# Kernel tuning notes

Hardware: AMD Instinct MI355X
Metric: run time of the kernel (lower is better)

## Reference

```python
import jax, jax.numpy as jnp
import numpy as np

DECAY = 0.8
EPS = 1e-05


def setup_inputs() -> dict:
    key = jax.random.key(0)
    k_x, k_e = jax.random.split(key)
    x = jax.random.normal(k_x, (8, 4096, 256), dtype=jnp.float32)
    embed = jax.random.normal(k_e, (8192, 256), dtype=jnp.float32)
    cluster_size = jnp.zeros((8192,), dtype=jnp.float32)
    embed_avg = embed  # buffer initialized as embed.clone()
    return {"x": x, "embed": embed, "cluster_size": cluster_size, "embed_avg": embed_avg}


def reference(x, embed, cluster_size, embed_avg):
    shape = x.shape
    K, d = embed.shape
    flatten = x.reshape(-1, d)  # [N, d]

    dist = -(jnp.sum(flatten * flatten, axis=1, keepdims=True)
             - 2.0 * (flatten @ embed.T)
             + jnp.sum(embed * embed, axis=1)[None, :])  # [N, K]
    embed_ind = jnp.argmax(dist, axis=-1)  # [N]

    quantize = jnp.take(embed, embed_ind, axis=0).reshape(shape)
    embed_ind_out = embed_ind.reshape(shape[:-1])

    # Training-mode EMA update (one_hot sum / one_hot matmul expressed as scatter-adds)
    counts = jnp.zeros((K,), dtype=x.dtype).at[embed_ind].add(1.0)  # embed_onehot.sum(0)
    embed_sum = jnp.zeros((K, d), dtype=x.dtype).at[embed_ind].add(flatten)  # (flatten^T @ onehot)^T

    new_cluster_size = cluster_size * DECAY + counts * (1.0 - DECAY)
    new_embed_avg = embed_avg * DECAY + embed_sum * (1.0 - DECAY)

    smoothed = (new_cluster_size + EPS) / (new_cluster_size.sum() + K * EPS) * new_cluster_size.sum()
    new_embed = new_embed_avg / smoothed[:, None]

    return quantize, embed_ind_out, new_cluster_size, new_embed_avg, new_embed
```

## Files before the change

kernel.cpp:

```cpp
#include <hip/hip_runtime.h>

#define N_ROWS 32768
#define DIM    256
#define KCODES 8192
#define DECAYF 0.8f
#define OMDF   0.2f
#define EPSF   1e-5f

#define Q_OFF    0
#define IND_OFF  8388608
#define CS_OFF   8421376
#define EA_OFF   8429568
#define NE_OFF   10526720


#define WS_E2    0
#define WS_CNT   8192
#define WS_START 16384
#define WS_CUR   24576
#define WS_SUM   40960

typedef _Float16 half8 __attribute__((ext_vector_type(8)));
typedef float floatx16 __attribute__((ext_vector_type(16)));

#define GLOAD16(g, l) __builtin_amdgcn_global_load_lds( \
    (const __attribute__((address_space(1))) void*)(g), \
    (__attribute__((address_space(3))) void*)(l), 16, 0, 0)

#define PREP_ROWS 32
__global__ void prep_all_kernel(const float* __restrict__ x,
                                const float* __restrict__ embed,
                                const float* __restrict__ cs,
                                _Float16* __restrict__ Xp,
                                _Float16* __restrict__ Ep,
                                float* __restrict__ out,
                                float* __restrict__ ws) {
  __shared__ __align__(16) _Float16 L[PREP_ROWS][264];
  __shared__ float red[4];
  const int t = threadIdx.x;
  const int bid = blockIdx.x;

  if (bid < 1024) {
    if (bid < 128) {
      unsigned long long* gbest = (unsigned long long*)(out + EA_OFF);
      gbest[bid * 256 + t] = 0ULL;
    } else if (bid < 160) {
      ((int*)(ws + WS_CNT))[(bid - 128) * 256 + t] = 0;
    }
    const int row0 = bid * PREP_ROWS;
    #pragma unroll
    for (int it = 0; it < 8; ++it) {
      int idx = it * 256 + t;
      int r = idx >> 6, q = idx & 63;
      float4 v = *(const float4*)&x[(size_t)(row0 + r) * DIM + q * 4];
      L[r][q * 4 + 0] = (_Float16)v.x;
      L[r][q * 4 + 1] = (_Float16)v.y;
      L[r][q * 4 + 2] = (_Float16)v.z;
      L[r][q * 4 + 3] = (_Float16)v.w;
    }
    __syncthreads();
    #pragma unroll
    for (int it = 0; it < 4; ++it) {
      int idx = it * 256 + t;
      int slot = idx >> 5, r = idx & 31;
      *(float4*)&Xp[((size_t)slot * N_ROWS + row0 + r) * 8] =
          *(const float4*)&L[r][slot * 8];
    }
  } else {
    const int row0 = (bid - 1024) * PREP_ROWS;
    float* e2 = ws + WS_E2;
    #pragma unroll
    for (int it = 0; it < 8; ++it) {
      int idx = it * 256 + t;
      int r = idx >> 6, q = idx & 63;
      float4 v = *(const float4*)&embed[(size_t)(row0 + r) * DIM + q * 4];
      L[r][q * 4 + 0] = (_Float16)v.x;
      L[r][q * 4 + 1] = (_Float16)v.y;
      L[r][q * 4 + 2] = (_Float16)v.z;
      L[r][q * 4 + 3] = (_Float16)v.w;
      float ssq = v.x * v.x + v.y * v.y + v.z * v.z + v.w * v.w;
      #pragma unroll
      for (int o = 32; o; o >>= 1) ssq += __shfl_xor(ssq, o);
      if ((t & 63) == 0) e2[row0 + r] = ssq;
    }
    if (bid == 1024) {
      float s = 0.0f;
      for (int j = t; j < KCODES; j += 256) s += cs[j];
      #pragma unroll
      for (int o = 32; o; o >>= 1) s += __shfl_xor(s, o);
      if ((t & 63) == 0) red[t >> 6] = s;
    }
    __syncthreads();
    if (bid == 1024 && t == 0)
      ws[WS_SUM] = red[0] + red[1] + red[2] + red[3];
    #pragma unroll
    for (int it = 0; it < 4; ++it) {
      int idx = it * 256 + t;
      int slot = idx >> 5, r = idx & 31;
      *(float4*)&Ep[((size_t)slot * KCODES + row0 + r) * 8] =
          *(const float4*)&L[r][slot * 8];
    }
  }
}

__global__ __launch_bounds__(512, 2) void main_kernel(
    const _Float16* __restrict__ Xp, const _Float16* __restrict__ Ep,
    const float* __restrict__ e2, unsigned long long* __restrict__ gbest) {
  __shared__ __align__(16) _Float16 As[4 * 4 * 256 * 8];
  __shared__ __align__(16) _Float16 Bs[4 * 4 * 256 * 8];
  __shared__ __align__(16) float e2s[256];

  const int t = threadIdx.x;
  const int w = t >> 6;
  const int lane = t & 63;
  const int l31 = lane & 31;
  const int h = lane >> 5;
  const int wm = w >> 2;
  const int wn = w & 3;

  const int bid = blockIdx.x;
  const int bi = bid >> 3;
  const int cb = (bid & 7) * 4 + (bi >> 5);
  const int rbg = bi & 31;
  const int codes0 = cb * 256;
  const int rowbase = rbg * 1024;

  const bool isA = (w < 4);
  const int slot = isA ? w : (w - 4);

  const _Float16* estage = Ep + ((size_t)slot * KCODES + codes0 + lane) * 8;
  const _Float16* xstage = Xp + ((size_t)slot * N_ROWS + rowbase + lane) * 8;
  _Float16* adst = &As[slot * 2048];
  _Float16* bdst = &Bs[slot * 2048];

  auto stage = [&](int s) {
    const int buf = s & 3;
    const int se4 = (s & 7) * 4;
    if (isA) {
      const _Float16* src = estage + (size_t)se4 * KCODES * 8;
      _Float16* dst = adst + buf * 8192;
      #pragma unroll
      for (int q = 0; q < 4; ++q)
        GLOAD16(src + q * 512, dst + q * 512);
    } else {
      const _Float16* src =
          xstage + (size_t)se4 * N_ROWS * 8 + (size_t)(s >> 3) * 256 * 8;
      _Float16* dst = bdst + buf * 8192;
      #pragma unroll
      for (int q = 0; q < 4; ++q)
        GLOAD16(src + q * 512, dst + q * 512);
    }
  };

  if (t < 64) {
    float4 v = *(const float4*)&e2[codes0 + t * 4];
    *(float4*)&e2s[t * 4] = v;
  }
  __builtin_amdgcn_sched_barrier(0);
  stage(0);
  stage(1);
  asm volatile("s_waitcnt vmcnt(4)" ::: "memory");
  asm volatile("s_waitcnt lgkmcnt(0)" ::: "memory");
  __builtin_amdgcn_s_barrier();
  __builtin_amdgcn_sched_barrier(0);

  floatx16 acc[4][2];
  unsigned long long pbest[4][2];

  #pragma unroll
  for (int tile = 0; tile < 4; ++tile) {
    #pragma unroll
    for (int ct = 0; ct < 4; ++ct) {
      const int cl = wm * 128 + ct * 32 + 4 * h;
      #pragma unroll
      for (int rq = 0; rq < 4; ++rq) {
        float4 v = *(const float4*)&e2s[cl + rq * 8];
        acc[ct][0][rq * 4 + 0] = -0.5f * v.x;
        acc[ct][0][rq * 4 + 1] = -0.5f * v.y;
        acc[ct][0][rq * 4 + 2] = -0.5f * v.z;
        acc[ct][0][rq * 4 + 3] = -0.5f * v.w;
      }
      acc[ct][1] = acc[ct][0];
    }

    #pragma unroll
    for (int i = 0; i < 8; ++i) {
      const int s = tile * 8 + i;
      if (s + 2 < 32) stage(s + 2);
      __builtin_amdgcn_sched_barrier(0);

      const int cur = (s & 3) * 8192;
      #pragma unroll
      for (int ks = 0; ks < 2; ++ks) {
        const int sbase = cur + (2 * ks + h) * 2048;
        half8 a0 = *(const half8*)&As[sbase + (wm * 128 + l31) * 8];
        half8 a1 = *(const half8*)&As[sbase + (wm * 128 + 32 + l31) * 8];
        half8 a2 = *(const half8*)&As[sbase + (wm * 128 + 64 + l31) * 8];
        half8 a3 = *(const half8*)&As[sbase + (wm * 128 + 96 + l31) * 8];
        half8 b0 = *(const half8*)&Bs[sbase + (wn * 64 + l31) * 8];
        half8 b1 = *(const half8*)&Bs[sbase + (wn * 64 + 32 + l31) * 8];
        __builtin_amdgcn_s_setprio(1);
        acc[0][0] = __builtin_amdgcn_mfma_f32_32x32x16_f16(a0, b0, acc[0][0], 0, 0, 0);
        acc[0][1] = __builtin_amdgcn_mfma_f32_32x32x16_f16(a0, b1, acc[0][1], 0, 0, 0);
        acc[1][0] = __builtin_amdgcn_mfma_f32_32x32x16_f16(a1, b0, acc[1][0], 0, 0, 0);
        acc[1][1] = __builtin_amdgcn_mfma_f32_32x32x16_f16(a1, b1, acc[1][1], 0, 0, 0);
        acc[2][0] = __builtin_amdgcn_mfma_f32_32x32x16_f16(a2, b0, acc[2][0], 0, 0, 0);
        acc[2][1] = __builtin_amdgcn_mfma_f32_32x32x16_f16(a2, b1, acc[2][1], 0, 0, 0);
        acc[3][0] = __builtin_amdgcn_mfma_f32_32x32x16_f16(a3, b0, acc[3][0], 0, 0, 0);
        acc[3][1] = __builtin_amdgcn_mfma_f32_32x32x16_f16(a3, b1, acc[3][1], 0, 0, 0);
        __builtin_amdgcn_s_setprio(0);
      }
      __builtin_amdgcn_sched_barrier(0);

      if (s < 31) {
        if (s < 30) {
          asm volatile("s_waitcnt vmcnt(4)" ::: "memory");
        } else {
          asm volatile("s_waitcnt vmcnt(0)" ::: "memory");
        }
        __builtin_amdgcn_s_barrier();
        __builtin_amdgcn_sched_barrier(0);
      }
    }

    #pragma unroll
    for (int rt = 0; rt < 2; ++rt) {
      float best = -3.0e38f;
      int bidx = 0;
      #pragma unroll
      for (int ct = 0; ct < 4; ++ct) {
        const int cbase = codes0 + wm * 128 + ct * 32 + 4 * h;
        #pragma unroll
        for (int r = 0; r < 16; ++r) {
          const int code = cbase + (r & 3) + 8 * (r >> 2);
          float v = acc[ct][rt][r];
          if (v > best || (v == best && code < bidx)) { best = v; bidx = code; }
        }
      }
      unsigned u = __float_as_uint(best);
      u = (u & 0x80000000u) ? ~u : (u | 0x80000000u);
      unsigned long long p =
          ((unsigned long long)u << 32) | (unsigned)(8191 - bidx);
      unsigned long long op = (unsigned long long)__shfl_xor((long long)p, 32);
      if (op > p) p = op;
      pbest[tile][rt] = p;
    }
  }

  #pragma unroll
  for (int tile = 0; tile < 4; ++tile)
    #pragma unroll
    for (int rt = 0; rt < 2; ++rt)
      if (h == 0)
        atomicMax(&gbest[rowbase + tile * 256 + wn * 64 + rt * 32 + l31],
                  pbest[tile][rt]);
}

__global__ void decode_count_kernel(const unsigned long long* __restrict__ gbest,
                                    float* __restrict__ out,
                                    int* __restrict__ cnt) {
  int r = blockIdx.x * blockDim.x + threadIdx.x;
  unsigned long long p = gbest[r];
  int k = 8191 - (int)(unsigned)(p & 0xFFFFFFFFull);
  out[IND_OFF + r] = (float)k;
  atomicAdd(&cnt[k], 1);
}

__global__ void prefix_kernel(const int* __restrict__ cnt,
                              int* __restrict__ start,
                              int* __restrict__ cursor) {
  __shared__ int part[1024];
  const int t = threadIdx.x;
  int loc[8];
  int s = 0;
  #pragma unroll
  for (int j = 0; j < 8; ++j) { loc[j] = cnt[t * 8 + j]; s += loc[j]; }
  part[t] = s;
  __syncthreads();
  for (int off = 1; off < 1024; off <<= 1) {
    int v = (t >= off) ? part[t - off] : 0;
    __syncthreads();
    part[t] += v;
    __syncthreads();
  }
  int base = part[t] - s;
  #pragma unroll
  for (int j = 0; j < 8; ++j) {
    start[t * 8 + j] = base;
    cursor[t * 8 + j] = base;
    base += loc[j];
  }
}

__global__ void scatter_rows_kernel(const float* __restrict__ out,
                                    int* __restrict__ cursor,
                                    int* __restrict__ rowlist) {
  int r = blockIdx.x * blockDim.x + threadIdx.x;
  int k = (int)out[IND_OFF + r];
  int pos = atomicAdd(&cursor[k], 1);
  rowlist[pos] = r;
}

__global__ void bucket_final_kernel(const float* __restrict__ x,
                                    const float* __restrict__ cs,
                                    const float* __restrict__ embed_avg,
                                    const int* __restrict__ start,
                                    const int* __restrict__ cnt,
                                    const int* __restrict__ rowlist,
                                    float* __restrict__ out,
                                    const float* __restrict__ ws_sum) {
  const int lane = threadIdx.x & 63;
  const int k = blockIdx.x * 4 + (threadIdx.x >> 6);
  const int s = start[k];
  const int n = cnt[k];
  float4 acc = make_float4(0.f, 0.f, 0.f, 0.f);
  int i = 0;
  for (; i + 2 <= n; i += 2) {
    int r0 = rowlist[s + i];
    int r1 = rowlist[s + i + 1];
    float4 v0 = *(const float4*)&x[(size_t)r0 * DIM + lane * 4];
    float4 v1 = *(const float4*)&x[(size_t)r1 * DIM + lane * 4];
    acc.x += v0.x + v1.x; acc.y += v0.y + v1.y;
    acc.z += v0.z + v1.z; acc.w += v0.w + v1.w;
  }
  if (i < n) {
    int r0 = rowlist[s + i];
    float4 v0 = *(const float4*)&x[(size_t)r0 * DIM + lane * 4];
    acc.x += v0.x; acc.y += v0.y; acc.z += v0.z; acc.w += v0.w;
  }
  const float S = DECAYF * (*ws_sum) + OMDF * (float)N_ROWS;
  const float scale = S / (S + (float)KCODES * EPSF);
  float ncs = cs[k] * DECAYF + (float)n * OMDF;
  if (lane == 0) out[CS_OFF + k] = ncs;
  float4 ea = *(const float4*)&embed_avg[(size_t)k * DIM + lane * 4];
  float4 nea;
  nea.x = ea.x * DECAYF + acc.x * OMDF;
  nea.y = ea.y * DECAYF + acc.y * OMDF;
  nea.z = ea.z * DECAYF + acc.z * OMDF;
  nea.w = ea.w * DECAYF + acc.w * OMDF;
  *(float4*)&out[EA_OFF + (size_t)k * DIM + lane * 4] = nea;
  float inv_sm = 1.0f / ((ncs + EPSF) * scale);
  float4 ne;
  ne.x = nea.x * inv_sm;
  ne.y = nea.y * inv_sm;
  ne.z = nea.z * inv_sm;
  ne.w = nea.w * inv_sm;
  *(float4*)&out[NE_OFF + (size_t)k * DIM + lane * 4] = ne;
}

__global__ void finish_q_kernel(const float* __restrict__ embed,
                                float* __restrict__ out) {
  const int lane = threadIdx.x & 63;
  const int wave = (blockIdx.x * blockDim.x + threadIdx.x) >> 6;
  for (int row = wave; row < N_ROWS; row += 2048) {
    int k = (int)out[IND_OFF + row];
    float4 ev = *(const float4*)&embed[(size_t)k * DIM + lane * 4];
    *(float4*)&out[Q_OFF + (size_t)row * DIM + lane * 4] = ev;
  }
}

extern "C" void kernel_launch(void* const* d_in, const int* in_sizes, int n_in,
                              void* d_out, int out_size, void* d_ws, size_t ws_size,
                              hipStream_t stream) {
  const float* x = (const float*)d_in[0];
  const float* embed = (const float*)d_in[1];
  const float* cs = (const float*)d_in[2];
  const float* ea = (const float*)d_in[3];
  float* out = (float*)d_out;
  float* ws = (float*)d_ws;

  float* e2 = ws + WS_E2;
  int* cnt = (int*)(ws + WS_CNT);
  int* start = (int*)(ws + WS_START);
  int* cursor = (int*)(ws + WS_CUR);
  float* ws_sum = ws + WS_SUM;

  _Float16* Xp = (_Float16*)(out + Q_OFF);
  int* rowlist = (int*)(out + Q_OFF + 4194304);
  unsigned long long* gbest = (unsigned long long*)(out + EA_OFF);
  _Float16* Ep = (_Float16*)(out + EA_OFF + 65536);

  prep_all_kernel<<<1280, 256, 0, stream>>>(x, embed, cs, Xp, Ep, out, ws);
  main_kernel<<<1024, 512, 0, stream>>>(Xp, Ep, e2, gbest);
  decode_count_kernel<<<128, 256, 0, stream>>>(gbest, out, cnt);
  prefix_kernel<<<1, 1024, 0, stream>>>(cnt, start, cursor);
  scatter_rows_kernel<<<128, 256, 0, stream>>>(out, cursor, rowlist);
  bucket_final_kernel<<<2048, 256, 0, stream>>>(x, cs, ea, start, cnt,
                                                rowlist, out, ws_sum);
  finish_q_kernel<<<512, 256, 0, stream>>>(embed, out);
}
```

Before: 378.5 us.

## Make distance GEMM blocks persistent over 4096 rows with a continuous prefetch pipeline

Each main_kernel block now covers 4096 rows (16 row tiles, processed in 4 super-groups) instead of 1024, and the grid shrinks from 1024 to 256 blocks. The staging lambda takes an explicit buffer, k-slice and row-tile, so the double-buffered global-to-LDS prefetch runs without a break across row tiles. Atomic argmax updates to gbest are flushed after each group of 4 tiles. The aim is to amortise block start-up costs and pipeline fill/drain, and to avoid a second dispatch wave. The cost is that with one block per CU the kernel runs at half of the allowed occupancy, which leaves fewer waves to hide memory latency.

```diff
diff --git a/kernel.cpp b/kernel.cpp
--- a/kernel.cpp
+++ b/kernel.cpp
@@ -120,10 +120,10 @@
 
   const int bid = blockIdx.x;
   const int bi = bid >> 3;
-  const int cb = (bid & 7) * 4 + (bi >> 5);
-  const int rbg = bi & 31;
+  const int cb = (bid & 7) * 4 + (bi >> 3);
+  const int rbg = bi & 7;
   const int codes0 = cb * 256;
-  const int rowbase = rbg * 1024;
+  const int rowbase = rbg * 4096;
 
   const bool isA = (w < 4);
   const int slot = isA ? w : (w - 4);
@@ -133,18 +133,16 @@
   _Float16* adst = &As[slot * 2048];
   _Float16* bdst = &Bs[slot * 2048];
 
-  auto stage = [&](int s) {
-    const int buf = s & 3;
-    const int se4 = (s & 7) * 4;
+  auto stage = [&](int buf, int se4, int rowT) {
     if (isA) {
-      const _Float16* src = estage + (size_t)se4 * KCODES * 8;
+      const _Float16* src = estage + (size_t)se4 * (KCODES * 8);
       _Float16* dst = adst + buf * 8192;
       #pragma unroll
       for (int q = 0; q < 4; ++q)
         GLOAD16(src + q * 512, dst + q * 512);
     } else {
       const _Float16* src =
-          xstage + (size_t)se4 * N_ROWS * 8 + (size_t)(s >> 3) * 256 * 8;
+          xstage + (size_t)se4 * (N_ROWS * 8) + (size_t)rowT * 2048;
       _Float16* dst = bdst + buf * 8192;
       #pragma unroll
       for (int q = 0; q < 4; ++q)
@@ -157,8 +155,8 @@
     *(float4*)&e2s[t * 4] = v;
   }
   __builtin_amdgcn_sched_barrier(0);
-  stage(0);
-  stage(1);
+  stage(0, 0, 0);
+  stage(1, 4, 0);
   asm volatile("s_waitcnt vmcnt(4)" ::: "memory");
   asm volatile("s_waitcnt lgkmcnt(0)" ::: "memory");
   __builtin_amdgcn_s_barrier();
@@ -167,93 +165,105 @@
   floatx16 acc[4][2];
   unsigned long long pbest[4][2];
 
-  #pragma unroll
-  for (int tile = 0; tile < 4; ++tile) {
-    #pragma unroll
-    for (int ct = 0; ct < 4; ++ct) {
-      const int cl = wm * 128 + ct * 32 + 4 * h;
-      #pragma unroll
-      for (int rq = 0; rq < 4; ++rq) {
-        float4 v = *(const float4*)&e2s[cl + rq * 8];
-        acc[ct][0][rq * 4 + 0] = -0.5f * v.x;
-        acc[ct][0][rq * 4 + 1] = -0.5f * v.y;
-        acc[ct][0][rq * 4 + 2] = -0.5f * v.z;
-        acc[ct][0][rq * 4 + 3] = -0.5f * v.w;
+  #pragma unroll 1
+  for (int sg = 0; sg < 4; ++sg) {
+    #pragma unroll
+    for (int tt = 0; tt < 4; ++tt) {
+      const int rowT = sg * 4 + tt;
+      #pragma unroll
+      for (int ct = 0; ct < 4; ++ct) {
+        const int cl = wm * 128 + ct * 32 + 4 * h;
+        #pragma unroll
+        for (int rq = 0; rq < 4; ++rq) {
+          float4 v = *(const float4*)&e2s[cl + rq * 8];
+          acc[ct][0][rq * 4 + 0] = -0.5f * v.x;
+          acc[ct][0][rq * 4 + 1] = -0.5f * v.y;
+          acc[ct][0][rq * 4 + 2] = -0.5f * v.z;
+          acc[ct][0][rq * 4 + 3] = -0.5f * v.w;
+        }
+        acc[ct][1] = acc[ct][0];
       }
-      acc[ct][1] = acc[ct][0];
-    }
-
-    #pragma unroll
-    for (int i = 0; i < 8; ++i) {
-      const int s = tile * 8 + i;
-      if (s + 2 < 32) stage(s + 2);
-      __builtin_amdgcn_sched_barrier(0);
-
-      const int cur = (s & 3) * 8192;
-      #pragma unroll
-      for (int ks = 0; ks < 2; ++ks) {
-        const int sbase = cur + (2 * ks + h) * 2048;
-        half8 a0 = *(const half8*)&As[sbase + (wm * 128 + l31) * 8];
-        half8 a1 = *(const half8*)&As[sbase + (wm * 128 + 32 + l31) * 8];
-        half8 a2 = *(const half8*)&As[sbase + (wm * 128 + 64 + l31) * 8];
-        half8 a3 = *(const half8*)&As[sbase + (wm * 128 + 96 + l31) * 8];
-        half8 b0 = *(const half8*)&Bs[sbase + (wn * 64 + l31) * 8];
-        half8 b1 = *(const half8*)&Bs[sbase + (wn * 64 + 32 + l31) * 8];
-        __builtin_amdgcn_s_setprio(1);
-        acc[0][0] = __builtin_amdgcn_mfma_f32_32x32x16_f16(a0, b0, acc[0][0], 0, 0, 0);
-        acc[0][1] = __builtin_amdgcn_mfma_f32_32x32x16_f16(a0, b1, acc[0][1], 0, 0, 0);
-        acc[1][0] = __builtin_amdgcn_mfma_f32_32x32x16_f16(a1, b0, acc[1][0], 0, 0, 0);
-        acc[1][1] = __builtin_amdgcn_mfma_f32_32x32x16_f16(a1, b1, acc[1][1], 0, 0, 0);
-        acc[2][0] = __builtin_amdgcn_mfma_f32_32x32x16_f16(a2, b0, acc[2][0], 0, 0, 0);
-        acc[2][1] = __builtin_amdgcn_mfma_f32_32x32x16_f16(a2, b1, acc[2][1], 0, 0, 0);
-        acc[3][0] = __builtin_amdgcn_mfma_f32_32x32x16_f16(a3, b0, acc[3][0], 0, 0, 0);
-        acc[3][1] = __builtin_amdgcn_mfma_f32_32x32x16_f16(a3, b1, acc[3][1], 0, 0, 0);
-        __builtin_amdgcn_s_setprio(0);
-      }
-      __builtin_amdgcn_sched_barrier(0);
-
-      if (s < 31) {
-        if (s < 30) {
-          asm volatile("s_waitcnt vmcnt(4)" ::: "memory");
-        } else {
-          asm volatile("s_waitcnt vmcnt(0)" ::: "memory");
+
+      #pragma unroll
+      for (int i = 0; i < 8; ++i) {
+        const bool lastTile = (sg == 3 && tt == 3);
+        if (!(lastTile && i >= 6)) {
+          const int ip = i + 2;
+          stage(ip & 3, (ip & 7) * 4, rowT + (ip >> 3));
         }
-        __builtin_amdgcn_s_barrier();
         __builtin_amdgcn_sched_barrier(0);
-      }
-    }
-
-    #pragma unroll
-    for (int rt = 0; rt < 2; ++rt) {
-      float best = -3.0e38f;
-      int bidx = 0;
-      #pragma unroll
-      for (int ct = 0; ct < 4; ++ct) {
-        const int cbase = codes0 + wm * 128 + ct * 32 + 4 * h;
+
+        const int cur = (i & 3) * 8192;
         #pragma unroll
-        for (int r = 0; r < 16; ++r) {
-          const int code = cbase + (r & 3) + 8 * (r >> 2);
-          float v = acc[ct][rt][r];
-          if (v > best || (v == best && code < bidx)) { best = v; bidx = code; }
+        for (int ks = 0; ks < 2; ++ks) {
+          const int sbase = cur + (2 * ks + h) * 2048;
+          half8 a0 = *(const half8*)&As[sbase + (wm * 128 + l31) * 8];
+          half8 a1 = *(const half8*)&As[sbase + (wm * 128 + 32 + l31) * 8];
+          half8 a2 = *(const half8*)&As[sbase + (wm * 128 + 64 + l31) * 8];
+          half8 a3 = *(const half8*)&As[sbase + (wm * 128 + 96 + l31) * 8];
+          half8 b0 = *(const half8*)&Bs[sbase + (wn * 64 + l31) * 8];
+          half8 b1 = *(const half8*)&Bs[sbase + (wn * 64 + 32 + l31) * 8];
+          __builtin_amdgcn_s_setprio(1);
+          acc[0][0] = __builtin_amdgcn_mfma_f32_32x32x16_f16(a0, b0, acc[0][0], 0, 0, 0);
+          acc[0][1] = __builtin_amdgcn_mfma_f32_32x32x16_f16(a0, b1, acc[0][1], 0, 0, 0);
+          acc[1][0] = __builtin_amdgcn_mfma_f32_32x32x16_f16(a1, b0, acc[1][0], 0, 0, 0);
+          acc[1][1] = __builtin_amdgcn_mfma_f32_32x32x16_f16(a1, b1, acc[1][1], 0, 0, 0);
+          acc[2][0] = __builtin_amdgcn_mfma_f32_32x32x16_f16(a2, b0, acc[2][0], 0, 0, 0);
+          acc[2][1] = __builtin_amdgcn_mfma_f32_32x32x16_f16(a2, b1, acc[2][1], 0, 0, 0);
+          acc[3][0] = __builtin_amdgcn_mfma_f32_32x32x16_f16(a3, b0, acc[3][0], 0, 0, 0);
+          acc[3][1] = __builtin_amdgcn_mfma_f32_32x32x16_f16(a3, b1, acc[3][1], 0, 0, 0);
+          __builtin_amdgcn_s_setprio(0);
+        }
+        __builtin_amdgcn_sched_barrier(0);
+
+        if (!(lastTile && i == 7)) {
+          if (!(lastTile && i == 6)) {
+            asm volatile("s_waitcnt vmcnt(4)" ::: "memory");
+          } else {
+            asm volatile("s_waitcnt vmcnt(0)" ::: "memory");
+          }
+          __builtin_amdgcn_s_barrier();
+          __builtin_amdgcn_sched_barrier(0);
         }
       }
-      unsigned u = __float_as_uint(best);
-      u = (u & 0x80000000u) ? ~u : (u | 0x80000000u);
-      unsigned long long p =
-          ((unsigned long long)u << 32) | (unsigned)(8191 - bidx);
-      unsigned long long op = (unsigned long long)__shfl_xor((long long)p, 32);
-      if (op > p) p = op;
-      pbest[tile][rt] = p;
-    }
-  }
-
-  #pragma unroll
-  for (int tile = 0; tile < 4; ++tile)
-    #pragma unroll
-    for (int rt = 0; rt < 2; ++rt)
-      if (h == 0)
-        atomicMax(&gbest[rowbase + tile * 256 + wn * 64 + rt * 32 + l31],
-                  pbest[tile][rt]);
+
+      #pragma unroll
+      for (int rt = 0; rt < 2; ++rt) {
+        float best = -3.0e38f;
+        int bidx = 0;
+        #pragma unroll
+        for (int ct = 0; ct < 4; ++ct) {
+          const int cbase = codes0 + wm * 128 + ct * 32 + 4 * h;
+          #pragma unroll
+          for (int r = 0; r < 16; ++r) {
+            const int code = cbase + (r & 3) + 8 * (r >> 2);
+            float v = acc[ct][rt][r];
+            if (v > best || (v == best && code < bidx)) { best = v; bidx = code; }
+          }
+        }
+        unsigned u = __float_as_uint(best);
+        u = (u & 0x80000000u) ? ~u : (u | 0x80000000u);
+        unsigned long long p =
+            ((unsigned long long)u << 32) | (unsigned)(8191 - bidx);
+        unsigned long long op = (unsigned long long)__shfl_xor((long long)p, 32);
+        if (op > p) p = op;
+        pbest[tt][rt] = p;
+      }
+    }
+
+    #pragma unroll
+    for (int tt2 = 0; tt2 < 4; ++tt2)
+      #pragma unroll
+      for (int rt = 0; rt < 2; ++rt)
+        if (h == 0)
+          atomicMax(&gbest[rowbase + (sg * 4 + tt2) * 256 + wn * 64 +
+                           rt * 32 + l31],
+                    pbest[tt2][rt]);
+    if (sg < 3) {
+      asm volatile("s_waitcnt vmcnt(0)" ::: "memory");
+      __builtin_amdgcn_sched_barrier(0);
+    }
+  }
 }
 
 __global__ void decode_count_kernel(const unsigned long long* __restrict__ gbest,
@@ -381,7 +391,7 @@
   _Float16* Ep = (_Float16*)(out + EA_OFF + 65536);
 
   prep_all_kernel<<<1280, 256, 0, stream>>>(x, embed, cs, Xp, Ep, out, ws);
-  main_kernel<<<1024, 512, 0, stream>>>(Xp, Ep, e2, gbest);
+  main_kernel<<<256, 512, 0, stream>>>(Xp, Ep, e2, gbest);
   decode_count_kernel<<<128, 256, 0, stream>>>(gbest, out, cnt);
   prefix_kernel<<<1, 1024, 0, stream>>>(cnt, start, cursor);
   scatter_rows_kernel<<<128, 256, 0, stream>>>(out, cursor, rowlist);
```

Result: no change. 379.1 us (+0.2%).
